# Performance work log

Measured on AMD Instinct MI355X. Metric: run time of the kernel, lower is better.

## Reference

```python
import jax, jax.numpy as jnp
import numpy as np

B = 512          # batch
V = 6890         # SMPL vertices
NB = 10          # num_betas
NJ = 24          # joints (root + 23 body)
# canonical SMPL kinematic tree (parents[0] = -1 for root)
PARENTS = np.array([-1,0,0,0,1,2,3,4,5,6,7,8,9,9,9,12,13,14,16,17,18,19,20,21], dtype=np.int32)


def rodrigues(rot_vecs):
    """Axis-angle [N,3] -> rotation matrices [N,3,3] (matches batch_rodrigues)."""
    angle = jnp.linalg.norm(rot_vecs + 1e-8, axis=1, keepdims=True)  # [N,1]
    rot_dir = rot_vecs / angle
    cos = jnp.cos(angle)[:, :, None]  # [N,1,1]
    sin = jnp.sin(angle)[:, :, None]
    rx, ry, rz = rot_dir[:, 0], rot_dir[:, 1], rot_dir[:, 2]
    zeros = jnp.zeros_like(rx)
    K = jnp.stack([zeros, -rz, ry,
                   rz, zeros, -rx,
                   -ry, rx, zeros], axis=1).reshape(-1, 3, 3)
    I = jnp.eye(3, dtype=rot_vecs.dtype)
    return I[None] + sin * K + (1.0 - cos) * jnp.matmul(K, K)


def setup_inputs() -> dict:
    key = jax.random.key(0)
    ks = jax.random.split(key, 8)
    betas = jnp.concatenate([jnp.ones((B, 1), jnp.float32),
                             0.5 * jax.random.normal(ks[0], (B, NB), jnp.float32)], axis=1)
    body_pose = 0.3 * jax.random.normal(ks[1], (B, 3 * (NJ - 1)), jnp.float32)
    global_orient = 0.3 * jax.random.normal(ks[2], (B, 3), jnp.float32)
    transl = jax.random.normal(ks[3], (B, 3), jnp.float32)
    shapedirs = 0.01 * jax.random.normal(ks[4], (V, 3, NB), jnp.float32)
    v_template = jax.random.normal(ks[5], (V, 3), jnp.float32)
    Jr = jax.random.uniform(ks[6], (NJ, V), jnp.float32)
    Jr = Jr / jnp.sum(Jr, axis=1, keepdims=True)
    W = jax.random.uniform(ks[7], (V, NJ), jnp.float32)
    W = W / jnp.sum(W, axis=1, keepdims=True)             # convex skinning weights
    return dict(betas=betas, body_pose=body_pose, global_orient=global_orient,
                transl=transl, shapedirs=shapedirs, v_template=v_template,
                J_regressor=Jr, lbs_weights=W)


def reference(betas, body_pose, global_orient, transl,
              shapedirs, v_template, J_regressor, lbs_weights):
    dt = v_template.dtype
    blend = jnp.einsum('bl,mkl->bmk', betas[:, 1:], shapedirs)            # [B,V,3]
    v_shaped = (v_template[None] + blend) * betas[:, 0][:, None, None]    # [B,V,3]
    J = jnp.einsum('bik,ji->bjk', v_shaped, J_regressor)                  # [B,NJ,3]
    # ---- updatePose: axis-angle -> rotmats
    full_pose = jnp.concatenate([global_orient, body_pose], axis=1)       # [B,NJ*3]
    rot_mats = rodrigues(full_pose.reshape(-1, 3)).reshape(-1, NJ, 3, 3)  # [B,NJ,3,3]
    # ---- kinematic chain (batch_rigid_transform)
    rel = J.at[:, 1:].add(-J[:, PARENTS[1:]])                             # rel joint offsets
    T_local = jnp.concatenate([rot_mats, rel[..., None]], axis=3)         # [B,NJ,3,4]
    bottom = jnp.broadcast_to(jnp.array([0, 0, 0, 1], dt), (rot_mats.shape[0], NJ, 1, 4))
    T_local = jnp.concatenate([T_local, bottom], axis=2)                  # [B,NJ,4,4]
    chain = [T_local[:, 0]]
    for i in range(1, NJ):  # fixed 24-node tree
        chain.append(jnp.matmul(chain[PARENTS[i]], T_local[:, i]))
    transforms = jnp.stack(chain, axis=1)                                 # [B,NJ,4,4]
    J_transformed = transforms[:, :, :3, 3]                               # [B,NJ,3]
    # relative transforms: subtract rotated rest joint from translation column
    init_t = jnp.einsum('bnij,bnj->bni', transforms[:, :, :3, :3], J)
    A = transforms.at[:, :, :3, 3].add(-init_t)                           # [B,NJ,4,4]
    # ---- skinning: T = W @ A, apply to homogeneous verts
    T = jnp.einsum('vn,bnij->bvij', lbs_weights, A)                       # [B,V,4,4]
    verts = (jnp.einsum('bvij,bvj->bvi', T[:, :, :3, :3], v_shaped)
             + T[:, :, :3, 3] + transl[:, None])                          # [B,V,3]
    return verts, J_transformed
```

## Files before the change

kernel.cpp:

```cpp
#include <hip/hip_runtime.h>

#define BATCH 512
#define V 6890
#define NJ 24
#define VH (V/2)

#define SD_N (V*30)
#define VT_N (V*3)
#define W_N  (V*24)
#define TOT_PK (SD_N+VT_N+W_N)
#define PREP_BLOCKS ((TOT_PK+255)/256)
#define NCH 8
#define JREG_BLOCKS (NJ*NCH)
#define CH_SZ ((V+NCH-1)/NCH)

#define A_OFF   0
#define BS_OFF  147456
#define JP_OFF  155648
#define PK_OFF  162048

__device__ const int d_par[NJ] = {-1,0,0,0,1,2,3,4,5,6,7,8,9,9,9,12,13,14,16,17,18,19,20,21};

__global__ __launch_bounds__(256) void prepjreg_k(
    const float* __restrict__ sd, const float* __restrict__ vt, const float* __restrict__ W,
    const float* __restrict__ Jr,
    float* __restrict__ dst, float* __restrict__ JP)
{
  __shared__ float red[4*33];
  const int bid = blockIdx.x;
  const int t = threadIdx.x;
  if (bid < PREP_BLOCKS){
    int i = bid*256 + t;
    if (i >= TOT_PK) return;
    float val;
    if (i < SD_N){ int j=i/V, v=i-j*V; val = sd[v*30+j]; }
    else if (i < SD_N+VT_N){ int o=i-SD_N; int j=o/V, v=o-j*V; val = vt[v*3+j]; }
    else { int o=i-SD_N-VT_N; int j=o/V, v=o-j*V; val = W[v*24+j]; }
    dst[i] = val;
    return;
  }
  const int r  = bid - PREP_BLOCKS;
  const int j  = r % NJ;
  const int v0 = (r / NJ)*CH_SZ;
  const int v1 = (v0+CH_SZ < V) ? v0+CH_SZ : V;
  float acc[33];
#pragma unroll
  for (int m=0;m<33;m++) acc[m]=0.f;
  for (int v=v0+t; v<v1; v+=256){
    const float jr = Jr[j*V+v];
    const float* __restrict__ vp = vt + v*3;
    acc[0] = fmaf(jr, vp[0], acc[0]);
    acc[1] = fmaf(jr, vp[1], acc[1]);
    acc[2] = fmaf(jr, vp[2], acc[2]);
    const float2* __restrict__ sp = (const float2*)(sd + v*30);
#pragma unroll
    for (int m=0;m<15;m++){
      const float2 s = sp[m];
      acc[3+2*m]   = fmaf(jr, s.x, acc[3+2*m]);
      acc[3+2*m+1] = fmaf(jr, s.y, acc[3+2*m+1]);
    }
  }
  const int lane = t & 63, wid = t >> 6;
#pragma unroll
  for (int m=0;m<33;m++){
    float x = acc[m];
    x += __shfl_xor(x, 1);
    x += __shfl_xor(x, 2);
    x += __shfl_xor(x, 4);
    x += __shfl_xor(x, 8);
    x += __shfl_xor(x, 16);
    x += __shfl_xor(x, 32);
    if (lane == 0) red[wid*33+m] = x;
  }
  __syncthreads();
  if (t < 33){
    JP[r*33 + t] = red[t] + red[33+t] + red[66+t] + red[99+t];
  }
}

__global__ __launch_bounds__(64) void batch_k(
    const float* __restrict__ betas, const float* __restrict__ body_pose,
    const float* __restrict__ go, const float* __restrict__ transl,
    const float* __restrict__ JP,
    float* __restrict__ A, float* __restrict__ bsc, float* __restrict__ jout)
{
  const int b = blockIdx.x;
  const int t = threadIdx.x;
  __shared__ float lb[11];
  __shared__ float lJ[72];
  __shared__ float lR[NJ*9];
  __shared__ float lL[NJ*12];
  __shared__ float lW[NJ*12];
  if (t < 11) lb[t] = betas[b*11+t];
  __syncthreads();
  const float b0 = lb[0];
  for (int idx=t; idx<72; idx+=64){
    const int j = idx/3, k = idx-3*j;
    float s = 0.f;
#pragma unroll
    for (int ch=0; ch<NCH; ch++){
      const float* __restrict__ jp = JP + (ch*NJ+j)*33;
      float ss = jp[k];
#pragma unroll
      for (int l=0;l<10;l++) ss = fmaf(lb[1+l], jp[3 + k*10 + l], ss);
      s += ss;
    }
    lJ[idx] = b0*s;
  }
  if (t==0) bsc[b*16] = b0;
  if (t>=1 && t<11) bsc[b*16+t] = b0*lb[t];
  if (t<3) bsc[b*16+11+t] = transl[b*3+t];
  if (t < NJ){
    float p0,p1,p2;
    if (t==0){ p0=go[b*3+0]; p1=go[b*3+1]; p2=go[b*3+2]; }
    else { int o=b*69+(t-1)*3; p0=body_pose[o]; p1=body_pose[o+1]; p2=body_pose[o+2]; }
    float a0=p0+1e-8f, a1=p1+1e-8f, a2=p2+1e-8f;
    float angle = sqrtf(a0*a0+a1*a1+a2*a2);
    float inv = 1.0f/angle;
    float rx=p0*inv, ry=p1*inv, rz=p2*inv;
    float sn = sinf(angle), cs = cosf(angle), mc = 1.0f-cs;
    float K[9] = {0.f,-rz,ry, rz,0.f,-rx, -ry,rx,0.f};
    float KK[9];
    #pragma unroll
    for (int r=0;r<3;r++)
      #pragma unroll
      for (int c=0;c<3;c++)
        KK[r*3+c] = K[r*3+0]*K[0+c] + K[r*3+1]*K[3+c] + K[r*3+2]*K[6+c];
    #pragma unroll
    for (int e=0;e<9;e++){
      float ident = (e==0||e==4||e==8)?1.0f:0.0f;
      lR[t*9+e] = ident + sn*K[e] + mc*KK[e];
    }
  }
  __syncthreads();
  for (int idx=t; idx<288; idx+=64){
    int j = idx/12, rc = idx-12*j, r = rc>>2, c = rc&3;
    float val;
    if (c<3) val = lR[j*9 + r*3 + c];
    else {
      int p = (j==0) ? 0 : d_par[j];
      val = (j==0) ? lJ[r] : (lJ[j*3+r] - lJ[p*3+r]);
    }
    lL[idx] = val;
  }
  __syncthreads();
  if (t<12) lW[t] = lL[t];
  __syncthreads();
  for (int i=1;i<NJ;i++){
    if (t<12){
      int p = d_par[i];
      int r = t>>2, c = t&3;
      float s = lW[p*12+r*4+0]*lL[i*12+0+c]
              + lW[p*12+r*4+1]*lL[i*12+4+c]
              + lW[p*12+r*4+2]*lL[i*12+8+c];
      if (c==3) s += lW[p*12+r*4+3];
      lW[i*12+t] = s;
    }
    __syncthreads();
  }
  for (int idx=t; idx<72; idx+=64){
    int j=idx/3, k=idx-3*j;
    jout[b*72+idx] = lW[j*12+k*4+3];
  }
  const int g = b>>1, q = b&1;
  float* __restrict__ Ab = A + g*576 + q*12;
  for (int idx=t; idx<288; idx+=64){
    int n=idx/12, rc=idx-12*n, r=rc>>2, c=rc&3;
    float val = lW[n*12+rc];
    if (c==3){
      val -= lW[n*12+r*4+0]*lJ[n*3+0] + lW[n*12+r*4+1]*lJ[n*3+1] + lW[n*12+r*4+2]*lJ[n*3+2];
    }
    Ab[n*24 + rc] = val;
  }
}

__global__ __launch_bounds__(256, 8) void main_k(
    const float* __restrict__ A, const float* __restrict__ bsc,
    const float2* __restrict__ pk, float* __restrict__ out)
{
  const int vh = blockIdx.x*256 + threadIdx.x;
  if (vh >= VH) return;
  const int bg = blockIdx.y;
  const float* __restrict__ Ag = A + bg*576;
  const float* __restrict__ bs = bsc + bg*32;

  const float2 vt0 = pk[30*VH + vh];
  const float2 vt1 = pk[31*VH + vh];
  const float2 vt2 = pk[32*VH + vh];

  float2 vs[2][3];
#pragma unroll
  for (int q=0;q<2;q++){
    const float b0 = bs[q*16];
    vs[q][0] = make_float2(b0*vt0.x, b0*vt0.y);
    vs[q][1] = make_float2(b0*vt1.x, b0*vt1.y);
    vs[q][2] = make_float2(b0*vt2.x, b0*vt2.y);
  }
#pragma unroll
  for (int l=0;l<10;l++){
    const float2 s0 = pk[(0*10+l)*VH + vh];
    const float2 s1 = pk[(1*10+l)*VH + vh];
    const float2 s2 = pk[(2*10+l)*VH + vh];
#pragma unroll
    for (int q=0;q<2;q++){
      const float c = bs[q*16+1+l];
      vs[q][0].x = fmaf(c, s0.x, vs[q][0].x); vs[q][0].y = fmaf(c, s0.y, vs[q][0].y);
      vs[q][1].x = fmaf(c, s1.x, vs[q][1].x); vs[q][1].y = fmaf(c, s1.y, vs[q][1].y);
      vs[q][2].x = fmaf(c, s2.x, vs[q][2].x); vs[q][2].y = fmaf(c, s2.y, vs[q][2].y);
    }
  }

  float y[2][6];
#pragma unroll
  for (int q=0;q<2;q++)
#pragma unroll
    for (int i=0;i<6;i++) y[q][i] = 0.f;

#pragma unroll 4
  for (int n=0;n<NJ;n++){
    const float2 w = pk[(33+n)*VH + vh];
#pragma unroll
    for (int q=0;q<2;q++){
      const float* __restrict__ an = Ag + n*24 + q*12;
      float tt;
      tt = fmaf(an[2], vs[q][2].x, fmaf(an[1], vs[q][1].x, fmaf(an[0], vs[q][0].x, an[3])));
      y[q][0] = fmaf(w.x, tt, y[q][0]);
      tt = fmaf(an[2], vs[q][2].y, fmaf(an[1], vs[q][1].y, fmaf(an[0], vs[q][0].y, an[3])));
      y[q][1] = fmaf(w.y, tt, y[q][1]);
      tt = fmaf(an[6], vs[q][2].x, fmaf(an[5], vs[q][1].x, fmaf(an[4], vs[q][0].x, an[7])));
      y[q][2] = fmaf(w.x, tt, y[q][2]);
      tt = fmaf(an[6], vs[q][2].y, fmaf(an[5], vs[q][1].y, fmaf(an[4], vs[q][0].y, an[7])));
      y[q][3] = fmaf(w.y, tt, y[q][3]);
      tt = fmaf(an[10], vs[q][2].x, fmaf(an[9], vs[q][1].x, fmaf(an[8], vs[q][0].x, an[11])));
      y[q][4] = fmaf(w.x, tt, y[q][4]);
      tt = fmaf(an[10], vs[q][2].y, fmaf(an[9], vs[q][1].y, fmaf(an[8], vs[q][0].y, an[11])));
      y[q][5] = fmaf(w.y, tt, y[q][5]);
    }
  }

  const int v0 = 2*vh;
#pragma unroll
  for (int q=0;q<2;q++){
    const float t0 = bs[q*16+11], t1 = bs[q*16+12], t2 = bs[q*16+13];
    const int b = bg*2 + q;
    float2* __restrict__ o2 = (float2*)(out + (b*V + v0)*3);
    o2[0] = make_float2(y[q][0]+t0, y[q][2]+t1);
    o2[1] = make_float2(y[q][4]+t2, y[q][1]+t0);
    o2[2] = make_float2(y[q][3]+t1, y[q][5]+t2);
  }
}

extern "C" void kernel_launch(void* const* d_in, const int* in_sizes, int n_in,
                              void* d_out, int out_size, void* d_ws, size_t ws_size,
                              hipStream_t stream)
{
  const float* betas     = (const float*)d_in[0];
  const float* body_pose = (const float*)d_in[1];
  const float* go        = (const float*)d_in[2];
  const float* transl    = (const float*)d_in[3];
  const float* sdirs     = (const float*)d_in[4];
  const float* vtempl    = (const float*)d_in[5];
  const float* Jr        = (const float*)d_in[6];
  const float* lw        = (const float*)d_in[7];
  float* wsf = (float*)d_ws;
  float* out = (float*)d_out;

  hipLaunchKernelGGL(prepjreg_k, dim3(PREP_BLOCKS + JREG_BLOCKS), dim3(256), 0, stream,
                     sdirs, vtempl, lw, Jr, wsf+PK_OFF, wsf+JP_OFF);
  hipLaunchKernelGGL(batch_k, dim3(BATCH), dim3(64), 0, stream,
                     betas, body_pose, go, transl, wsf+JP_OFF,
                     wsf+A_OFF, wsf+BS_OFF, out + BATCH*V*3);
  hipLaunchKernelGGL(main_k, dim3((VH+255)/256, BATCH/2), dim3(256), 0, stream,
                     wsf+A_OFF, wsf+BS_OFF, (const float2*)(wsf+PK_OFF), out);
}
```

Baseline: 144.3 us.

## Fuse per-batch transform chain into skinning kernel with LDS-resident transforms

Merges the per-batch kinematic-chain kernel into the main skinning kernel. Each block recomputes the joint transforms for its two batch elements in shared memory and then skins two vertex tiles, so the A/bsc workspace round trip and one launch go away. The cost is redundant work: the serial 23-step chain with a barrier per step is recomputed by each of the 7 blocks in a batch group. Grid shrinks to 7x256 blocks, with each thread handling two tiles.

```diff
diff --git a/kernel.cpp b/kernel.cpp
--- a/kernel.cpp
+++ b/kernel.cpp
@@ -14,10 +14,8 @@
 #define JREG_BLOCKS (NJ*NCH)
 #define CH_SZ ((V+NCH-1)/NCH)
 
-#define A_OFF   0
-#define BS_OFF  147456
-#define JP_OFF  155648
-#define PK_OFF  162048
+#define JP_OFF  0
+#define PK_OFF  8192
 
 __device__ const int d_par[NJ] = {-1,0,0,0,1,2,3,4,5,6,7,8,9,9,9,12,13,14,16,17,18,19,20,21};
 
@@ -78,175 +76,190 @@
   }
 }
 
-__global__ __launch_bounds__(64) void batch_k(
+__global__ __launch_bounds__(256, 8) void fused_k(
     const float* __restrict__ betas, const float* __restrict__ body_pose,
     const float* __restrict__ go, const float* __restrict__ transl,
-    const float* __restrict__ JP,
-    float* __restrict__ A, float* __restrict__ bsc, float* __restrict__ jout)
+    const float* __restrict__ JP, const float2* __restrict__ pk,
+    float* __restrict__ out, float* __restrict__ jout)
 {
-  const int b = blockIdx.x;
-  const int t = threadIdx.x;
-  __shared__ float lb[11];
-  __shared__ float lJ[72];
-  __shared__ float lR[NJ*9];
-  __shared__ float lL[NJ*12];
-  __shared__ float lW[NJ*12];
-  if (t < 11) lb[t] = betas[b*11+t];
-  __syncthreads();
-  const float b0 = lb[0];
-  for (int idx=t; idx<72; idx+=64){
-    const int j = idx/3, k = idx-3*j;
+  const int t  = threadIdx.x;
+  const int ht = t & 127;
+  const int q  = t >> 7;
+  const int bg = blockIdx.y;
+  const int b  = bg*2 + q;
+
+  __shared__ float lb[2][11];
+  __shared__ float lJ[2][72];
+  __shared__ float lL[2][NJ*12];
+  __shared__ float lW[2][NJ*12];
+  __shared__ float lA[NJ*24];
+
+  if (ht < 11) lb[q][ht] = betas[b*11 + ht];
+  __syncthreads();
+
+  if (ht < 72){
+    const int j = ht/3, k = ht-3*j;
     float s = 0.f;
 #pragma unroll
     for (int ch=0; ch<NCH; ch++){
       const float* __restrict__ jp = JP + (ch*NJ+j)*33;
       float ss = jp[k];
 #pragma unroll
-      for (int l=0;l<10;l++) ss = fmaf(lb[1+l], jp[3 + k*10 + l], ss);
+      for (int l=0;l<10;l++) ss = fmaf(lb[q][1+l], jp[3 + k*10 + l], ss);
       s += ss;
     }
-    lJ[idx] = b0*s;
-  }
-  if (t==0) bsc[b*16] = b0;
-  if (t>=1 && t<11) bsc[b*16+t] = b0*lb[t];
-  if (t<3) bsc[b*16+11+t] = transl[b*3+t];
-  if (t < NJ){
+    lJ[q][ht] = lb[q][0]*s;
+  }
+  __syncthreads();
+
+  if (ht < NJ){
+    const int j = ht;
     float p0,p1,p2;
-    if (t==0){ p0=go[b*3+0]; p1=go[b*3+1]; p2=go[b*3+2]; }
-    else { int o=b*69+(t-1)*3; p0=body_pose[o]; p1=body_pose[o+1]; p2=body_pose[o+2]; }
+    if (j==0){ p0=go[b*3+0]; p1=go[b*3+1]; p2=go[b*3+2]; }
+    else { int o=b*69+(j-1)*3; p0=body_pose[o]; p1=body_pose[o+1]; p2=body_pose[o+2]; }
     float a0=p0+1e-8f, a1=p1+1e-8f, a2=p2+1e-8f;
     float angle = sqrtf(a0*a0+a1*a1+a2*a2);
     float inv = 1.0f/angle;
     float rx=p0*inv, ry=p1*inv, rz=p2*inv;
     float sn = sinf(angle), cs = cosf(angle), mc = 1.0f-cs;
     float K[9] = {0.f,-rz,ry, rz,0.f,-rx, -ry,rx,0.f};
-    float KK[9];
-    #pragma unroll
+    float R[9];
+#pragma unroll
     for (int r=0;r<3;r++)
-      #pragma unroll
-      for (int c=0;c<3;c++)
-        KK[r*3+c] = K[r*3+0]*K[0+c] + K[r*3+1]*K[3+c] + K[r*3+2]*K[6+c];
-    #pragma unroll
-    for (int e=0;e<9;e++){
-      float ident = (e==0||e==4||e==8)?1.0f:0.0f;
-      lR[t*9+e] = ident + sn*K[e] + mc*KK[e];
-    }
-  }
-  __syncthreads();
-  for (int idx=t; idx<288; idx+=64){
-    int j = idx/12, rc = idx-12*j, r = rc>>2, c = rc&3;
-    float val;
-    if (c<3) val = lR[j*9 + r*3 + c];
-    else {
-      int p = (j==0) ? 0 : d_par[j];
-      val = (j==0) ? lJ[r] : (lJ[j*3+r] - lJ[p*3+r]);
-    }
-    lL[idx] = val;
-  }
-  __syncthreads();
-  if (t<12) lW[t] = lL[t];
+#pragma unroll
+      for (int c=0;c<3;c++){
+        float kk = K[r*3+0]*K[0+c] + K[r*3+1]*K[3+c] + K[r*3+2]*K[6+c];
+        float ident = (r==c)?1.0f:0.0f;
+        R[r*3+c] = ident + sn*K[r*3+c] + mc*kk;
+      }
+    const int p = d_par[j];
+    float* __restrict__ row = &lL[q][j*12];
+    row[0]=R[0]; row[1]=R[1]; row[2]=R[2];
+    row[4]=R[3]; row[5]=R[4]; row[6]=R[5];
+    row[8]=R[6]; row[9]=R[7]; row[10]=R[8];
+    row[3]  = (j==0) ? lJ[q][0] : lJ[q][j*3+0] - lJ[q][p*3+0];
+    row[7]  = (j==0) ? lJ[q][1] : lJ[q][j*3+1] - lJ[q][p*3+1];
+    row[11] = (j==0) ? lJ[q][2] : lJ[q][j*3+2] - lJ[q][p*3+2];
+  }
+  __syncthreads();
+
+  if (ht < 12) lW[q][ht] = lL[q][ht];
   __syncthreads();
   for (int i=1;i<NJ;i++){
-    if (t<12){
-      int p = d_par[i];
-      int r = t>>2, c = t&3;
-      float s = lW[p*12+r*4+0]*lL[i*12+0+c]
-              + lW[p*12+r*4+1]*lL[i*12+4+c]
-              + lW[p*12+r*4+2]*lL[i*12+8+c];
-      if (c==3) s += lW[p*12+r*4+3];
-      lW[i*12+t] = s;
+    if (ht < 12){
+      const int p = d_par[i];
+      const int r = ht>>2, c = ht&3;
+      float s = lW[q][p*12+r*4+0]*lL[q][i*12+0+c]
+              + lW[q][p*12+r*4+1]*lL[q][i*12+4+c]
+              + lW[q][p*12+r*4+2]*lL[q][i*12+8+c];
+      if (c==3) s += lW[q][p*12+r*4+3];
+      lW[q][i*12+ht] = s;
     }
     __syncthreads();
   }
-  for (int idx=t; idx<72; idx+=64){
-    int j=idx/3, k=idx-3*j;
-    jout[b*72+idx] = lW[j*12+k*4+3];
-  }
-  const int g = b>>1, q = b&1;
-  float* __restrict__ Ab = A + g*576 + q*12;
-  for (int idx=t; idx<288; idx+=64){
-    int n=idx/12, rc=idx-12*n, r=rc>>2, c=rc&3;
-    float val = lW[n*12+rc];
+
+  if (blockIdx.x == 0 && ht < 72){
+    const int j = ht/3, k = ht-3*j;
+    jout[b*72 + ht] = lW[q][j*12 + k*4 + 3];
+  }
+
+  for (int idx=t; idx<NJ*24; idx+=256){
+    const int n = idx/24, rem = idx-24*n, qq = rem/12, rc = rem-12*qq;
+    const int r = rc>>2, c = rc&3;
+    float val = lW[qq][n*12+rc];
     if (c==3){
-      val -= lW[n*12+r*4+0]*lJ[n*3+0] + lW[n*12+r*4+1]*lJ[n*3+1] + lW[n*12+r*4+2]*lJ[n*3+2];
-    }
-    Ab[n*24 + rc] = val;
-  }
-}
-
-__global__ __launch_bounds__(256, 8) void main_k(
-    const float* __restrict__ A, const float* __restrict__ bsc,
-    const float2* __restrict__ pk, float* __restrict__ out)
-{
-  const int vh = blockIdx.x*256 + threadIdx.x;
-  if (vh >= VH) return;
-  const int bg = blockIdx.y;
-  const float* __restrict__ Ag = A + bg*576;
-  const float* __restrict__ bs = bsc + bg*32;
-
-  const float2 vt0 = pk[30*VH + vh];
-  const float2 vt1 = pk[31*VH + vh];
-  const float2 vt2 = pk[32*VH + vh];
-
-  float2 vs[2][3];
-#pragma unroll
-  for (int q=0;q<2;q++){
-    const float b0 = bs[q*16];
-    vs[q][0] = make_float2(b0*vt0.x, b0*vt0.y);
-    vs[q][1] = make_float2(b0*vt1.x, b0*vt1.y);
-    vs[q][2] = make_float2(b0*vt2.x, b0*vt2.y);
-  }
-#pragma unroll
-  for (int l=0;l<10;l++){
-    const float2 s0 = pk[(0*10+l)*VH + vh];
-    const float2 s1 = pk[(1*10+l)*VH + vh];
-    const float2 s2 = pk[(2*10+l)*VH + vh];
-#pragma unroll
-    for (int q=0;q<2;q++){
-      const float c = bs[q*16+1+l];
-      vs[q][0].x = fmaf(c, s0.x, vs[q][0].x); vs[q][0].y = fmaf(c, s0.y, vs[q][0].y);
-      vs[q][1].x = fmaf(c, s1.x, vs[q][1].x); vs[q][1].y = fmaf(c, s1.y, vs[q][1].y);
-      vs[q][2].x = fmaf(c, s2.x, vs[q][2].x); vs[q][2].y = fmaf(c, s2.y, vs[q][2].y);
-    }
-  }
-
-  float y[2][6];
-#pragma unroll
-  for (int q=0;q<2;q++)
-#pragma unroll
-    for (int i=0;i<6;i++) y[q][i] = 0.f;
+      val -= lW[qq][n*12+r*4+0]*lJ[qq][n*3+0]
+           + lW[qq][n*12+r*4+1]*lJ[qq][n*3+1]
+           + lW[qq][n*12+r*4+2]*lJ[qq][n*3+2];
+    }
+    lA[n*24 + qq*12 + rc] = val;
+  }
+  __syncthreads();
+
+  float b0s[2], cf[2][10], tr[2][3];
+#pragma unroll
+  for (int qq=0;qq<2;qq++){
+    const float* __restrict__ bp = betas + (bg*2+qq)*11;
+    const float bb0 = bp[0];
+    b0s[qq] = bb0;
+#pragma unroll
+    for (int l=0;l<10;l++) cf[qq][l] = bb0*bp[1+l];
+    const float* __restrict__ tp = transl + (bg*2+qq)*3;
+    tr[qq][0]=tp[0]; tr[qq][1]=tp[1]; tr[qq][2]=tp[2];
+  }
+
+#pragma unroll
+  for (int uu=0; uu<2; uu++){
+    const int vhtile = blockIdx.x + uu*7;
+    const int vh = vhtile*256 + t;
+    if (vh < VH){
+      const float2 vt0 = pk[30*VH + vh];
+      const float2 vt1 = pk[31*VH + vh];
+      const float2 vt2 = pk[32*VH + vh];
+
+      float2 vs[2][3];
+#pragma unroll
+      for (int qq=0;qq<2;qq++){
+        const float b0 = b0s[qq];
+        vs[qq][0] = make_float2(b0*vt0.x, b0*vt0.y);
+        vs[qq][1] = make_float2(b0*vt1.x, b0*vt1.y);
+        vs[qq][2] = make_float2(b0*vt2.x, b0*vt2.y);
+      }
+#pragma unroll
+      for (int l=0;l<10;l++){
+        const float2 s0 = pk[(0*10+l)*VH + vh];
+        const float2 s1 = pk[(1*10+l)*VH + vh];
+        const float2 s2 = pk[(2*10+l)*VH + vh];
+#pragma unroll
+        for (int qq=0;qq<2;qq++){
+          const float c = cf[qq][l];
+          vs[qq][0].x = fmaf(c, s0.x, vs[qq][0].x); vs[qq][0].y = fmaf(c, s0.y, vs[qq][0].y);
+          vs[qq][1].x = fmaf(c, s1.x, vs[qq][1].x); vs[qq][1].y = fmaf(c, s1.y, vs[qq][1].y);
+          vs[qq][2].x = fmaf(c, s2.x, vs[qq][2].x); vs[qq][2].y = fmaf(c, s2.y, vs[qq][2].y);
+        }
+      }
+
+      float y[2][6];
+#pragma unroll
+      for (int qq=0;qq<2;qq++)
+#pragma unroll
+        for (int i=0;i<6;i++) y[qq][i] = 0.f;
 
 #pragma unroll 4
-  for (int n=0;n<NJ;n++){
-    const float2 w = pk[(33+n)*VH + vh];
-#pragma unroll
-    for (int q=0;q<2;q++){
-      const float* __restrict__ an = Ag + n*24 + q*12;
-      float tt;
-      tt = fmaf(an[2], vs[q][2].x, fmaf(an[1], vs[q][1].x, fmaf(an[0], vs[q][0].x, an[3])));
-      y[q][0] = fmaf(w.x, tt, y[q][0]);
-      tt = fmaf(an[2], vs[q][2].y, fmaf(an[1], vs[q][1].y, fmaf(an[0], vs[q][0].y, an[3])));
-      y[q][1] = fmaf(w.y, tt, y[q][1]);
-      tt = fmaf(an[6], vs[q][2].x, fmaf(an[5], vs[q][1].x, fmaf(an[4], vs[q][0].x, an[7])));
-      y[q][2] = fmaf(w.x, tt, y[q][2]);
-      tt = fmaf(an[6], vs[q][2].y, fmaf(an[5], vs[q][1].y, fmaf(an[4], vs[q][0].y, an[7])));
-      y[q][3] = fmaf(w.y, tt, y[q][3]);
-      tt = fmaf(an[10], vs[q][2].x, fmaf(an[9], vs[q][1].x, fmaf(an[8], vs[q][0].x, an[11])));
-      y[q][4] = fmaf(w.x, tt, y[q][4]);
-      tt = fmaf(an[10], vs[q][2].y, fmaf(an[9], vs[q][1].y, fmaf(an[8], vs[q][0].y, an[11])));
-      y[q][5] = fmaf(w.y, tt, y[q][5]);
-    }
-  }
-
-  const int v0 = 2*vh;
-#pragma unroll
-  for (int q=0;q<2;q++){
-    const float t0 = bs[q*16+11], t1 = bs[q*16+12], t2 = bs[q*16+13];
-    const int b = bg*2 + q;
-    float2* __restrict__ o2 = (float2*)(out + (b*V + v0)*3);
-    o2[0] = make_float2(y[q][0]+t0, y[q][2]+t1);
-    o2[1] = make_float2(y[q][4]+t2, y[q][1]+t0);
-    o2[2] = make_float2(y[q][3]+t1, y[q][5]+t2);
+      for (int n=0;n<NJ;n++){
+        const float2 w = pk[(33+n)*VH + vh];
+#pragma unroll
+        for (int qq=0;qq<2;qq++){
+          const float4 A0 = *(const float4*)&lA[n*24+qq*12+0];
+          const float4 A1 = *(const float4*)&lA[n*24+qq*12+4];
+          const float4 A2 = *(const float4*)&lA[n*24+qq*12+8];
+          float tt;
+          tt = fmaf(A0.z, vs[qq][2].x, fmaf(A0.y, vs[qq][1].x, fmaf(A0.x, vs[qq][0].x, A0.w)));
+          y[qq][0] = fmaf(w.x, tt, y[qq][0]);
+          tt = fmaf(A0.z, vs[qq][2].y, fmaf(A0.y, vs[qq][1].y, fmaf(A0.x, vs[qq][0].y, A0.w)));
+          y[qq][1] = fmaf(w.y, tt, y[qq][1]);
+          tt = fmaf(A1.z, vs[qq][2].x, fmaf(A1.y, vs[qq][1].x, fmaf(A1.x, vs[qq][0].x, A1.w)));
+          y[qq][2] = fmaf(w.x, tt, y[qq][2]);
+          tt = fmaf(A1.z, vs[qq][2].y, fmaf(A1.y, vs[qq][1].y, fmaf(A1.x, vs[qq][0].y, A1.w)));
+          y[qq][3] = fmaf(w.y, tt, y[qq][3]);
+          tt = fmaf(A2.z, vs[qq][2].x, fmaf(A2.y, vs[qq][1].x, fmaf(A2.x, vs[qq][0].x, A2.w)));
+          y[qq][4] = fmaf(w.x, tt, y[qq][4]);
+          tt = fmaf(A2.z, vs[qq][2].y, fmaf(A2.y, vs[qq][1].y, fmaf(A2.x, vs[qq][0].y, A2.w)));
+          y[qq][5] = fmaf(w.y, tt, y[qq][5]);
+        }
+      }
+
+      const int v0 = 2*vh;
+#pragma unroll
+      for (int qq=0;qq<2;qq++){
+        const float t0 = tr[qq][0], t1 = tr[qq][1], t2 = tr[qq][2];
+        const int bb = bg*2 + qq;
+        float2* __restrict__ o2 = (float2*)(out + (bb*V + v0)*3);
+        o2[0] = make_float2(y[qq][0]+t0, y[qq][2]+t1);
+        o2[1] = make_float2(y[qq][4]+t2, y[qq][1]+t0);
+        o2[2] = make_float2(y[qq][3]+t1, y[qq][5]+t2);
+      }
+    }
   }
 }
 
@@ -267,9 +280,7 @@
 
   hipLaunchKernelGGL(prepjreg_k, dim3(PREP_BLOCKS + JREG_BLOCKS), dim3(256), 0, stream,
                      sdirs, vtempl, lw, Jr, wsf+PK_OFF, wsf+JP_OFF);
-  hipLaunchKernelGGL(batch_k, dim3(BATCH), dim3(64), 0, stream,
+  hipLaunchKernelGGL(fused_k, dim3(7, 256), dim3(256), 0, stream,
                      betas, body_pose, go, transl, wsf+JP_OFF,
-                     wsf+A_OFF, wsf+BS_OFF, out + BATCH*V*3);
-  hipLaunchKernelGGL(main_k, dim3((VH+255)/256, BATCH/2), dim3(256), 0, stream,
-                     wsf+A_OFF, wsf+BS_OFF, (const float2*)(wsf+PK_OFF), out);
+                     (const float2*)(wsf+PK_OFF), out, out + BATCH*V*3);
 }
```

Result: slower. 414.8 us (+187.5%).
